# Performance work log

Measured on AMD Instinct MI355X. Metric: run time of the kernel, lower is better.

## Reference

```python
import jax, jax.numpy as jnp
import numpy as np

B, S, H = 4, 256, 768
F = 32            # num_features
T = 256           # TAG_HIDDEN_SIZE
WD = 64           # WIDTH_HIDDEN_SIZE
C = 16            # num_tags


def setup_inputs() -> dict:
    key = jax.random.key(0)
    ks = jax.random.split(key, 10)
    inp = {
        "final_hidden": jax.random.normal(ks[0], (B, S, H), jnp.float32),
        "feature_vecs": jax.random.normal(ks[1], (B, S, F), jnp.float32),
        # Linear params stored [in, out] (transposed vs torch; same math)
        "start_W": jax.random.normal(ks[2], (H + F, T), jnp.float32) * (1.0 / np.sqrt(H + F)),
        "start_b": jnp.zeros((T,), jnp.float32),
        "end_W": jax.random.normal(ks[3], (H + F, T), jnp.float32) * (1.0 / np.sqrt(H + F)),
        "end_b": jnp.zeros((T,), jnp.float32),
        "U": jax.random.normal(ks[4], (T, C, T), jnp.float32) * (1.0 / np.sqrt(T)),
        "width_hidden": jax.random.uniform(ks[5], (S, S, WD), jnp.float32),
        "lin_W": jax.random.normal(ks[6], (2 * T + WD, C), jnp.float32) * (1.0 / np.sqrt(2 * T + WD)),
        "lin_b": jnp.zeros((C,), jnp.float32),
    }
    return inp


def reference(final_hidden, feature_vecs, start_W, start_b, end_W, end_b, U, width_hidden, lin_W, lin_b):
    # dropout p=0.0 -> identity
    x = jnp.concatenate([final_hidden, feature_vecs], axis=-1)   # [B,S,H+F]
    s = x @ start_W + start_b                                    # [B,S,T]
    e = x @ end_W + end_b                                        # [B,S,T]

    # biaffine term: einsum('bsh,hci->bsci') then ('bsci,bei->bsec')
    sU = jnp.einsum('bst,tcu->bscu', s, U)                       # [B,S,C,T]
    pre = jnp.einsum('bscu,beu->bsec', sU, e)                    # [B,S,S,C]

    # pairwise FFN, fused: Linear over concat(start, end, width) decomposes
    # into three small matmuls + broadcast adds (same math, no O(S^2*(2T+W)) buffer)
    Ws, We, Ww = lin_W[:T], lin_W[T:2 * T], lin_W[2 * T:]
    ffn = (jnp.einsum('bst,tc->bsc', s, Ws)[:, :, None, :]
           + jnp.einsum('bet,tc->bec', e, We)[:, None, :, :]
           + jnp.einsum('sew,wc->sec', width_hidden, Ww)[None]
           + lin_b)                                              # [B,S,S,C]
    return pre + ffn
```

## Files before the change

### kernel.cpp

```cpp
#include <hip/hip_runtime.h>


#define B_ 4
#define S_ 256
#define H_ 768
#define F_ 32
#define T_ 256
#define C_ 16
#define R_ 1024
#define HF 800

typedef unsigned short u16;
typedef __attribute__((ext_vector_type(8))) short short8;
typedef __attribute__((ext_vector_type(4))) float f32x4;

__device__ __forceinline__ u16 f2b(float x) {
    unsigned u = __builtin_bit_cast(unsigned, x);
    u += 0x7FFF + ((u >> 16) & 1);
    return (u16)(u >> 16);
}
__device__ __forceinline__ float b2f(u16 b) {
    unsigned u = ((unsigned)b) << 16;
    return __builtin_bit_cast(float, u);
}
__device__ __forceinline__ short8 cvt8(float4 a, float4 b) {
    short8 r;
    r[0] = (short)f2b(a.x); r[1] = (short)f2b(a.y);
    r[2] = (short)f2b(a.z); r[3] = (short)f2b(a.w);
    r[4] = (short)f2b(b.x); r[5] = (short)f2b(b.y);
    r[6] = (short)f2b(b.z); r[7] = (short)f2b(b.w);
    return r;
}

template<int K, int LDA, int LDB, int MF, int NF, int UNROLL>
__device__ __forceinline__ void core(const u16* __restrict__ A,
                                     const u16* __restrict__ B,
                                     int lr, int kgl, f32x4 acc[MF][NF])
{
    const u16* ap[MF];
    const u16* bp[NF];
#pragma unroll
    for (int i = 0; i < MF; ++i) ap[i] = A + (size_t)(i * 16 + lr) * LDA + kgl * 8;
#pragma unroll
    for (int j = 0; j < NF; ++j) bp[j] = B + (size_t)(j * 16 + lr) * LDB + kgl * 8;

#pragma unroll UNROLL
    for (int k = 0; k < K; k += 32) {
        short8 a[MF], b[NF];
#pragma unroll
        for (int i = 0; i < MF; ++i) a[i] = *(const short8*)(ap[i] + k);
#pragma unroll
        for (int j = 0; j < NF; ++j) b[j] = *(const short8*)(bp[j] + k);
#pragma unroll
        for (int i = 0; i < MF; ++i)
#pragma unroll
            for (int j = 0; j < NF; ++j)
                acc[i][j] = __builtin_amdgcn_mfma_f32_16x16x32_bf16(a[i], b[j], acc[i][j], 0, 0, 0);
    }
}

__global__ __launch_bounds__(256)
void k_cvtw(const float* __restrict__ sW, const float* __restrict__ eW,
            u16* __restrict__ Wt)
{
    __shared__ float t_[32][33];
    const int bid = blockIdx.x;
    const int tid = threadIdx.x;
    int k0 = (bid / 16) * 32;
    int j0 = (bid % 16) * 32;
    const float* src = (j0 < T_) ? sW : eW;
    const int js = (j0 < T_) ? j0 : j0 - T_;
    {
        int jl = tid & 31, kl0 = (tid >> 5) * 4;
#pragma unroll
        for (int i = 0; i < 4; ++i)
            t_[kl0 + i][jl] = src[(k0 + kl0 + i) * T_ + js + jl];
    }
    __syncthreads();
    {
        int kl = tid & 31, jl0 = (tid >> 5) * 4;
#pragma unroll
        for (int i = 0; i < 4; ++i)
            Wt[(size_t)(j0 + jl0 + i) * HF + k0 + kl] = f2b(t_[kl][jl0 + i]);
    }
}

__global__ __launch_bounds__(256)
void k_se_cvtu_wc(const float* __restrict__ fh, const float* __restrict__ fv,
                  const u16* __restrict__ Wt,
                  const float* __restrict__ sb, const float* __restrict__ eb,
                  const float* __restrict__ U,
                  const float* __restrict__ linW, const float* __restrict__ linb,
                  const float* __restrict__ WH,
                  u16* __restrict__ SEb, u16* __restrict__ Ut,
                  float* __restrict__ WC)
{
    const int bid = blockIdx.x;
    const int tid = threadIdx.x;

    if (bid < 128) {
        const int l = tid & 63, w = tid >> 6;
        const int wr = w >> 1, wc = w & 1;
        const int lr = l & 15, kgl = l >> 4;
        const int bm = (bid >> 4) * 64;
        const int bn = (bid & 15) * 64;
        f32x4 acc[2][2] = {};

        const u16* aw0 = Wt + (size_t)(bm + wr * 32 + lr) * HF + kgl * 8;
        const u16* aw1 = aw0 + (size_t)16 * HF;
        const float* xr0 = fh + (size_t)(bn + wc * 32 + lr) * H_ + kgl * 8;
        const float* xr1 = xr0 + (size_t)16 * H_;

#pragma unroll 4
        for (int k = 0; k < 768; k += 32) {
            short8 a0 = *(const short8*)(aw0 + k);
            short8 a1 = *(const short8*)(aw1 + k);
            float4 p0 = *(const float4*)(xr0 + k);
            float4 p1 = *(const float4*)(xr0 + k + 4);
            float4 q0 = *(const float4*)(xr1 + k);
            float4 q1 = *(const float4*)(xr1 + k + 4);
            short8 b0 = cvt8(p0, p1);
            short8 b1 = cvt8(q0, q1);
            acc[0][0] = __builtin_amdgcn_mfma_f32_16x16x32_bf16(a0, b0, acc[0][0], 0, 0, 0);
            acc[0][1] = __builtin_amdgcn_mfma_f32_16x16x32_bf16(a0, b1, acc[0][1], 0, 0, 0);
            acc[1][0] = __builtin_amdgcn_mfma_f32_16x16x32_bf16(a1, b0, acc[1][0], 0, 0, 0);
            acc[1][1] = __builtin_amdgcn_mfma_f32_16x16x32_bf16(a1, b1, acc[1][1], 0, 0, 0);
        }
        {
            short8 a0 = *(const short8*)(aw0 + 768);
            short8 a1 = *(const short8*)(aw1 + 768);
            const float* v0 = fv + (size_t)(bn + wc * 32 + lr) * F_ + kgl * 8;
            const float* v1 = v0 + (size_t)16 * F_;
            short8 b0 = cvt8(*(const float4*)v0, *(const float4*)(v0 + 4));
            short8 b1 = cvt8(*(const float4*)v1, *(const float4*)(v1 + 4));
            acc[0][0] = __builtin_amdgcn_mfma_f32_16x16x32_bf16(a0, b0, acc[0][0], 0, 0, 0);
            acc[0][1] = __builtin_amdgcn_mfma_f32_16x16x32_bf16(a0, b1, acc[0][1], 0, 0, 0);
            acc[1][0] = __builtin_amdgcn_mfma_f32_16x16x32_bf16(a1, b0, acc[1][0], 0, 0, 0);
            acc[1][1] = __builtin_amdgcn_mfma_f32_16x16x32_bf16(a1, b1, acc[1][1], 0, 0, 0);
        }

#pragma unroll
        for (int i = 0; i < 2; ++i) {
            int j0 = bm + wr * 32 + i * 16 + kgl * 4;
            float4 bias = (j0 < T_) ? *(const float4*)&sb[j0]
                                    : *(const float4*)&eb[j0 - T_];
#pragma unroll
            for (int jj = 0; jj < 2; ++jj) {
                int r = bn + wc * 32 + jj * 16 + lr;
                ushort4 o;
                o.x = f2b(acc[i][jj][0] + bias.x);
                o.y = f2b(acc[i][jj][1] + bias.y);
                o.z = f2b(acc[i][jj][2] + bias.z);
                o.w = f2b(acc[i][jj][3] + bias.w);
                *(ushort4*)&SEb[(size_t)r * 512 + j0] = o;
            }
        }
        return;
    }
    if (bid < 1152) {
        __shared__ float t_[32][33];
        int bid2 = bid - 128;
        int cu0 = (bid2 >> 3) * 32;
        int t0  = (bid2 & 7) * 32;
        {
            int cul = tid & 31, tl0 = (tid >> 5) * 4;
#pragma unroll
            for (int i = 0; i < 4; ++i)
                t_[tl0 + i][cul] = U[(size_t)(t0 + tl0 + i) * 4096 + cu0 + cul];
        }
        __syncthreads();
        {
            int tl = tid & 31, cul0 = (tid >> 5) * 4;
#pragma unroll
            for (int i = 0; i < 4; ++i)
                Ut[(size_t)(cu0 + cul0 + i) * T_ + t0 + tl] = f2b(t_[tl][cul0 + i]);
        }
        return;
    }
    {
        __shared__ float Wl[16][64];
        __shared__ float Wwl[64][16];
        const int se0 = (bid - 1152) * 128;
        {
            int w0 = tid >> 2, c4 = tid & 3;
            *(float4*)&Wwl[w0][c4 * 4] = *(const float4*)&linW[(512 + w0) * 16 + c4 * 4];
        }
        const int sel = tid >> 4, c = tid & 15;
        const float lb = linb[c];
#pragma unroll
        for (int it = 0; it < 8; ++it) {
            __syncthreads();
            {
                int w4 = tid & 15;
                *(float4*)&Wl[sel][w4 * 4] =
                    *(const float4*)&WH[(size_t)(se0 + it * 16 + sel) * 64 + w4 * 4];
            }
            __syncthreads();
            float acc = lb;
#pragma unroll
            for (int w0 = 0; w0 < 64; ++w0)
                acc += Wl[sel][w0] * Wwl[w0][c];
            WC[(size_t)(se0 + it * 16 + sel) * 16 + c] = acc;
        }
    }
}

__global__ __launch_bounds__(256)
void k_su_scec(const u16* __restrict__ SEb, const u16* __restrict__ Ut,
               const float* __restrict__ linW,
               u16* __restrict__ SUb, float* __restrict__ SCEC)
{
    const int bid = blockIdx.x;
    const int tid = threadIdx.x;

    if (bid < 256) {
        const int l = tid & 63, w = tid >> 6;
        const int wcu = w & 1, wr2 = w >> 1;
        const int lr = l & 15, kgl = l >> 4;
        const int bm = (bid & 31) * 128;
        const int bn = (bid >> 5) * 128;
        f32x4 acc[4][4] = {};

        core<T_, T_, 512, 4, 4, 2>(Ut + (size_t)(bm + wcu * 64) * T_,
                                   SEb + (size_t)(bn + wr2 * 64) * 512,
                                   lr, kgl, acc);

#pragma unroll
        for (int i = 0; i < 4; ++i) {
            int cu0 = bm + wcu * 64 + i * 16 + kgl * 4;
#pragma unroll
            for (int j = 0; j < 4; ++j) {
                int r = bn + wr2 * 64 + j * 16 + lr;
                ushort4 o;
                o.x = f2b(acc[i][j][0]); o.y = f2b(acc[i][j][1]);
                o.z = f2b(acc[i][j][2]); o.w = f2b(acc[i][j][3]);
                *(ushort4*)&SUb[(size_t)r * 4096 + cu0] = o;
            }
        }
        return;
    }
    {
        __shared__ float SEl[4][512];
        const int r0 = (bid - 256) * 4;
#pragma unroll
        for (int i = 0; i < 2; ++i) {
            int ch = tid + i * 256;
            int rl = ch >> 7, o4 = (ch & 127) * 4;
            ushort4 v = *(const ushort4*)&SEb[(size_t)(r0 + rl) * 512 + o4];
            SEl[rl][o4 + 0] = b2f(v.x); SEl[rl][o4 + 1] = b2f(v.y);
            SEl[rl][o4 + 2] = b2f(v.z); SEl[rl][o4 + 3] = b2f(v.w);
        }
        __syncthreads();
        const int rl = tid >> 6, tq = (tid >> 4) & 3, c = tid & 15;
        const int t0 = tq * 64;
        float accs = 0.f, acce = 0.f;
#pragma unroll 4
        for (int t = t0; t < t0 + 64; ++t) {
            accs += SEl[rl][t]       * linW[t * 16 + c];
            acce += SEl[rl][256 + t] * linW[(256 + t) * 16 + c];
        }
        accs += __shfl_xor(accs, 16); accs += __shfl_xor(accs, 32);
        acce += __shfl_xor(acce, 16); acce += __shfl_xor(acce, 32);
        if (tq == 0) {
            SCEC[(r0 + rl) * 32 + c]      = accs;
            SCEC[(r0 + rl) * 32 + 16 + c] = acce;
        }
    }
}

__global__ __launch_bounds__(256)
void k_pre(const u16* __restrict__ SEb, const u16* __restrict__ SUb,
           const float* __restrict__ SCEC, const float* __restrict__ WC,
           float* __restrict__ OUT)
{
    const int bid = blockIdx.x;
    const int tid = threadIdx.x;
    const int n_idx = bid >> 3;
    const int b  = (bid >> 1) & 3;
    const int e_idx = bid & 1;
    const int bm = n_idx * 64;
    const int bn = e_idx * 128;
    const int l = tid & 63, w = tid >> 6;
    const int wn = w >> 1, we = w & 1;
    const int lr = l & 15, kgl = l >> 4;
    f32x4 acc[2][4] = {};

    const u16* An = SUb + ((size_t)b << 20) + (size_t)(bm + wn * 32) * T_;
    const u16* Be = SEb + (size_t)(b << 8) * 512 + 256 + (size_t)(bn + we * 64) * 512;

    core<T_, T_, 512, 2, 4, 4>(An, Be, lr, kgl, acc);

    const int c0 = kgl * 4;
#pragma unroll
    for (int i = 0; i < 2; ++i) {
        int n0 = bm + wn * 32 + i * 16;
        int s = n0 >> 4;
        float4 scv = *(const float4*)&SCEC[((b << 8) + s) * 32 + c0];
#pragma unroll
        for (int j = 0; j < 4; ++j) {
            int e = bn + we * 64 + j * 16 + lr;
            float4 ecv = *(const float4*)&SCEC[((b << 8) + e) * 32 + 16 + c0];
            float4 wcv = *(const float4*)&WC[(size_t)(s * S_ + e) * 16 + c0];
            float4 o;
            o.x = acc[i][j][0] + scv.x + ecv.x + wcv.x;
            o.y = acc[i][j][1] + scv.y + ecv.y + wcv.y;
            o.z = acc[i][j][2] + scv.z + ecv.z + wcv.z;
            o.w = acc[i][j][3] + scv.w + ecv.w + wcv.w;
            *(float4*)&OUT[(((size_t)(b << 8) + s) * S_ + e) * 16 + c0] = o;
        }
    }
}

extern "C" void kernel_launch(void* const* d_in, const int* in_sizes, int n_in,
                              void* d_out, int out_size, void* d_ws, size_t ws_size,
                              hipStream_t stream)
{
    const float* fh   = (const float*)d_in[0];
    const float* fv   = (const float*)d_in[1];
    const float* sW   = (const float*)d_in[2];
    const float* sb   = (const float*)d_in[3];
    const float* eW   = (const float*)d_in[4];
    const float* eb   = (const float*)d_in[5];
    const float* U    = (const float*)d_in[6];
    const float* WH   = (const float*)d_in[7];
    const float* linW = (const float*)d_in[8];
    const float* linb = (const float*)d_in[9];
    float* OUT = (float*)d_out;

    char* p = (char*)d_ws;
    u16* SUb = (u16*)p;      p += (size_t)B_ * 4096 * 256 * 2;
    float* WC = (float*)p;   p += (size_t)S_ * S_ * C_ * 4;
    u16* Ut  = (u16*)p;      p += (size_t)4096 * T_ * 2;
    u16* Wt  = (u16*)p;      p += (size_t)512 * HF * 2;
    u16* SEb = (u16*)p;      p += (size_t)R_ * 512 * 2;
    float* SCEC = (float*)p; p += (size_t)R_ * 32 * 4;

    k_cvtw<<<dim3(400), 256, 0, stream>>>(sW, eW, Wt);
    k_se_cvtu_wc<<<dim3(1664), 256, 0, stream>>>(fh, fv, Wt, sb, eb, U,
                                                 linW, linb, WH, SEb, Ut, WC);
    k_su_scec<<<dim3(512), 256, 0, stream>>>(SEb, Ut, linW, SUb, SCEC);
    k_pre<<<dim3(512), 256, 0, stream>>>(SEb, SUb, SCEC, WC, OUT);
}
```

Before: 62.01 us.

## Fuse weight transpose-convert into projection GEMM and interleave SU/SCEC blocks

Removes the separate k_cvtw launch that transposed and converted start/end weights to bf16. The projection GEMM now reads the fp32 weights directly with strided scalar loads and converts them in registers. It also interleaves the SU GEMM blocks and the SCEC blocks by block-index parity so the heavy and light work mix across the GPU instead of running in two separate phases. This saves a kernel launch and a workspace round trip, at the cost of uncoalesced strided weight loads inside the GEMM inner loop.

```diff
diff --git a/kernel.cpp b/kernel.cpp
--- a/kernel.cpp
+++ b/kernel.cpp
@@ -8,7 +8,6 @@
 #define T_ 256
 #define C_ 16
 #define R_ 1024
-#define HF 800
 
 typedef unsigned short u16;
 typedef __attribute__((ext_vector_type(8))) short short8;
@@ -31,6 +30,12 @@
     r[6] = (short)f2b(b.z); r[7] = (short)f2b(b.w);
     return r;
 }
+__device__ __forceinline__ short8 cvt8p(const float* t) {
+    short8 r;
+#pragma unroll
+    for (int i = 0; i < 8; ++i) r[i] = (short)f2b(t[i]);
+    return r;
+}
 
 template<int K, int LDA, int LDB, int MF, int NF, int UNROLL>
 __device__ __forceinline__ void core(const u16* __restrict__ A,
@@ -60,34 +65,8 @@
 }
 
 __global__ __launch_bounds__(256)
-void k_cvtw(const float* __restrict__ sW, const float* __restrict__ eW,
-            u16* __restrict__ Wt)
-{
-    __shared__ float t_[32][33];
-    const int bid = blockIdx.x;
-    const int tid = threadIdx.x;
-    int k0 = (bid / 16) * 32;
-    int j0 = (bid % 16) * 32;
-    const float* src = (j0 < T_) ? sW : eW;
-    const int js = (j0 < T_) ? j0 : j0 - T_;
-    {
-        int jl = tid & 31, kl0 = (tid >> 5) * 4;
-#pragma unroll
-        for (int i = 0; i < 4; ++i)
-            t_[kl0 + i][jl] = src[(k0 + kl0 + i) * T_ + js + jl];
-    }
-    __syncthreads();
-    {
-        int kl = tid & 31, jl0 = (tid >> 5) * 4;
-#pragma unroll
-        for (int i = 0; i < 4; ++i)
-            Wt[(size_t)(j0 + jl0 + i) * HF + k0 + kl] = f2b(t_[kl][jl0 + i]);
-    }
-}
-
-__global__ __launch_bounds__(256)
 void k_se_cvtu_wc(const float* __restrict__ fh, const float* __restrict__ fv,
-                  const u16* __restrict__ Wt,
+                  const float* __restrict__ sW, const float* __restrict__ eW,
                   const float* __restrict__ sb, const float* __restrict__ eb,
                   const float* __restrict__ U,
                   const float* __restrict__ linW, const float* __restrict__ linb,
@@ -106,19 +85,28 @@
         const int bn = (bid & 15) * 64;
         f32x4 acc[2][2] = {};
 
-        const u16* aw0 = Wt + (size_t)(bm + wr * 32 + lr) * HF + kgl * 8;
-        const u16* aw1 = aw0 + (size_t)16 * HF;
+        const float* srcW = (bm < T_) ? sW : eW;
+        const int js = (bm < T_) ? bm : bm - T_;
+        const int jA0 = js + wr * 32 + lr;
+        const int jA1 = jA0 + 16;
         const float* xr0 = fh + (size_t)(bn + wc * 32 + lr) * H_ + kgl * 8;
         const float* xr1 = xr0 + (size_t)16 * H_;
 
-#pragma unroll 4
-        for (int k = 0; k < 768; k += 32) {
-            short8 a0 = *(const short8*)(aw0 + k);
-            short8 a1 = *(const short8*)(aw1 + k);
-            float4 p0 = *(const float4*)(xr0 + k);
-            float4 p1 = *(const float4*)(xr0 + k + 4);
-            float4 q0 = *(const float4*)(xr1 + k);
-            float4 q1 = *(const float4*)(xr1 + k + 4);
+#pragma unroll 2
+        for (int k0 = 0; k0 < 768; k0 += 32) {
+            float t0[8], t1[8];
+#pragma unroll
+            for (int i = 0; i < 8; ++i) {
+                int krow = k0 + kgl * 8 + i;
+                t0[i] = srcW[(size_t)krow * T_ + jA0];
+                t1[i] = srcW[(size_t)krow * T_ + jA1];
+            }
+            short8 a0 = cvt8p(t0);
+            short8 a1 = cvt8p(t1);
+            float4 p0 = *(const float4*)(xr0 + k0);
+            float4 p1 = *(const float4*)(xr0 + k0 + 4);
+            float4 q0 = *(const float4*)(xr1 + k0);
+            float4 q1 = *(const float4*)(xr1 + k0 + 4);
             short8 b0 = cvt8(p0, p1);
             short8 b1 = cvt8(q0, q1);
             acc[0][0] = __builtin_amdgcn_mfma_f32_16x16x32_bf16(a0, b0, acc[0][0], 0, 0, 0);
@@ -127,8 +115,15 @@
             acc[1][1] = __builtin_amdgcn_mfma_f32_16x16x32_bf16(a1, b1, acc[1][1], 0, 0, 0);
         }
         {
-            short8 a0 = *(const short8*)(aw0 + 768);
-            short8 a1 = *(const short8*)(aw1 + 768);
+            float t0[8], t1[8];
+#pragma unroll
+            for (int i = 0; i < 8; ++i) {
+                int krow = 768 + kgl * 8 + i;
+                t0[i] = srcW[(size_t)krow * T_ + jA0];
+                t1[i] = srcW[(size_t)krow * T_ + jA1];
+            }
+            short8 a0 = cvt8p(t0);
+            short8 a1 = cvt8p(t1);
             const float* v0 = fv + (size_t)(bn + wc * 32 + lr) * F_ + kgl * 8;
             const float* v1 = v0 + (size_t)16 * F_;
             short8 b0 = cvt8(*(const float4*)v0, *(const float4*)(v0 + 4));
@@ -213,12 +208,13 @@
     const int bid = blockIdx.x;
     const int tid = threadIdx.x;
 
-    if (bid < 256) {
+    if (!(bid & 1)) {
+        const int idx = bid >> 1;
         const int l = tid & 63, w = tid >> 6;
         const int wcu = w & 1, wr2 = w >> 1;
         const int lr = l & 15, kgl = l >> 4;
-        const int bm = (bid & 31) * 128;
-        const int bn = (bid >> 5) * 128;
+        const int bm = (idx & 31) * 128;
+        const int bn = (idx >> 5) * 128;
         f32x4 acc[4][4] = {};
 
         core<T_, T_, 512, 4, 4, 2>(Ut + (size_t)(bm + wcu * 64) * T_,
@@ -241,7 +237,7 @@
     }
     {
         __shared__ float SEl[4][512];
-        const int r0 = (bid - 256) * 4;
+        const int r0 = (bid >> 1) * 4;
 #pragma unroll
         for (int i = 0; i < 2; ++i) {
             int ch = tid + i * 256;
@@ -331,12 +327,10 @@
     u16* SUb = (u16*)p;      p += (size_t)B_ * 4096 * 256 * 2;
     float* WC = (float*)p;   p += (size_t)S_ * S_ * C_ * 4;
     u16* Ut  = (u16*)p;      p += (size_t)4096 * T_ * 2;
-    u16* Wt  = (u16*)p;      p += (size_t)512 * HF * 2;
     u16* SEb = (u16*)p;      p += (size_t)R_ * 512 * 2;
     float* SCEC = (float*)p; p += (size_t)R_ * 32 * 4;
 
-    k_cvtw<<<dim3(400), 256, 0, stream>>>(sW, eW, Wt);
-    k_se_cvtu_wc<<<dim3(1664), 256, 0, stream>>>(fh, fv, Wt, sb, eb, U,
+    k_se_cvtu_wc<<<dim3(1664), 256, 0, stream>>>(fh, fv, sW, eW, sb, eb, U,
                                                  linW, linb, WH, SEb, Ut, WC);
     k_su_scec<<<dim3(512), 256, 0, stream>>>(SEb, Ut, linW, SUb, SCEC);
     k_pre<<<dim3(512), 256, 0, stream>>>(SEb, SUb, SCEC, WC, OUT);
```

Result: slower. 65.10 us (+5.0%).

## Merge four kernel launches into one persistent kernel with grid barriers

Applied to the files above, without the earlier changes.

Combines the weight-convert, projection, SU/SCEC and final biaffine stages into a single persistent kernel of 512 blocks separated by atomic-counter grid barriers, with the old conversion blocks distributed as a job loop. The goal is to remove per-launch overhead and inter-kernel gaps. In exchange it adds a memset launch, spin-wait barriers that require all 512 blocks to be co-resident, and it leaves some blocks idle during the stages with fewer work items.

```diff
diff --git a/kernel.cpp b/kernel.cpp
--- a/kernel.cpp
+++ b/kernel.cpp
@@ -9,8 +9,10 @@
 #define C_ 16
 #define R_ 1024
 #define HF 800
+#define NBLK 512
 
 typedef unsigned short u16;
+typedef unsigned int u32;
 typedef __attribute__((ext_vector_type(8))) short short8;
 typedef __attribute__((ext_vector_type(4))) float f32x4;
 
@@ -32,6 +34,25 @@
     return r;
 }
 
+__device__ __forceinline__ void gbar(u32* bar, int idx, int nb) {
+    __syncthreads();
+    if (threadIdx.x == 0) {
+        u32* cnt = bar + idx * 64;
+        u32* flg = bar + idx * 64 + 32;
+        __threadfence();
+        u32 old = atomicAdd(cnt, 1u);
+        if (old == (u32)(nb - 1)) {
+            __threadfence();
+            __hip_atomic_store(flg, 1u, __ATOMIC_RELAXED, __HIP_MEMORY_SCOPE_AGENT);
+        } else {
+            while (__hip_atomic_load(flg, __ATOMIC_RELAXED, __HIP_MEMORY_SCOPE_AGENT) == 0u)
+                __builtin_amdgcn_s_sleep(8);
+            __threadfence();
+        }
+    }
+    __syncthreads();
+}
+
 template<int K, int LDA, int LDB, int MF, int NF, int UNROLL>
 __device__ __forceinline__ void core(const u16* __restrict__ A,
                                      const u16* __restrict__ B,
@@ -59,44 +80,104 @@
     }
 }
 
-__global__ __launch_bounds__(256)
-void k_cvtw(const float* __restrict__ sW, const float* __restrict__ eW,
-            u16* __restrict__ Wt)
-{
-    __shared__ float t_[32][33];
+__device__ void cvtw_job(int job, int tid, const float* __restrict__ sW,
+                         const float* __restrict__ eW, u16* __restrict__ Wt,
+                         float* sh)
+{
+    float (*t_)[33] = (float(*)[33])sh;
+    int k0 = (job / 16) * 32;
+    int j0 = (job % 16) * 32;
+    const float* src = (j0 < T_) ? sW : eW;
+    const int js = (j0 < T_) ? j0 : j0 - T_;
+    {
+        int jl = tid & 31, kl0 = (tid >> 5) * 4;
+#pragma unroll
+        for (int i = 0; i < 4; ++i)
+            t_[kl0 + i][jl] = src[(k0 + kl0 + i) * T_ + js + jl];
+    }
+    __syncthreads();
+    {
+        int kl = tid & 31, jl0 = (tid >> 5) * 4;
+#pragma unroll
+        for (int i = 0; i < 4; ++i)
+            Wt[(size_t)(j0 + jl0 + i) * HF + k0 + kl] = f2b(t_[kl][jl0 + i]);
+    }
+    __syncthreads();
+}
+
+__device__ void cvtu_job(int job, int tid, const float* __restrict__ U,
+                         u16* __restrict__ Ut, float* sh)
+{
+    float (*t_)[33] = (float(*)[33])sh;
+    int cu0 = (job >> 3) * 32;
+    int t0  = (job & 7) * 32;
+    {
+        int cul = tid & 31, tl0 = (tid >> 5) * 4;
+#pragma unroll
+        for (int i = 0; i < 4; ++i)
+            t_[tl0 + i][cul] = U[(size_t)(t0 + tl0 + i) * 4096 + cu0 + cul];
+    }
+    __syncthreads();
+    {
+        int tl = tid & 31, cul0 = (tid >> 5) * 4;
+#pragma unroll
+        for (int i = 0; i < 4; ++i)
+            Ut[(size_t)(cu0 + cul0 + i) * T_ + t0 + tl] = f2b(t_[tl][cul0 + i]);
+    }
+    __syncthreads();
+}
+
+__device__ void wc_job(int job, int tid, const float* __restrict__ WH,
+                       const float* __restrict__ linW, const float* __restrict__ linb,
+                       float* __restrict__ WC, float* sh)
+{
+    float* Wl  = sh;
+    float* Wwl = sh + 1024;
+    const int se0 = job * 128;
+    {
+        int w0 = tid >> 2, c4 = tid & 3;
+        *(float4*)&Wwl[w0 * 16 + c4 * 4] = *(const float4*)&linW[(512 + w0) * 16 + c4 * 4];
+    }
+    const int sel = tid >> 4, c = tid & 15;
+    const float lb = linb[c];
+#pragma unroll
+    for (int it = 0; it < 8; ++it) {
+        __syncthreads();
+        {
+            int w4 = tid & 15;
+            *(float4*)&Wl[sel * 64 + w4 * 4] =
+                *(const float4*)&WH[(size_t)(se0 + it * 16 + sel) * 64 + w4 * 4];
+        }
+        __syncthreads();
+        float acc = lb;
+#pragma unroll
+        for (int w0 = 0; w0 < 64; ++w0)
+            acc += Wl[sel * 64 + w0] * Wwl[w0 * 16 + c];
+        WC[(size_t)(se0 + it * 16 + sel) * 16 + c] = acc;
+    }
+    __syncthreads();
+}
+
+__global__ __launch_bounds__(256, 2)
+void k_mega(const float* __restrict__ fh, const float* __restrict__ fv,
+            const float* __restrict__ sW, const float* __restrict__ sb,
+            const float* __restrict__ eW, const float* __restrict__ eb,
+            const float* __restrict__ U,  const float* __restrict__ WH,
+            const float* __restrict__ linW, const float* __restrict__ linb,
+            u16* __restrict__ Wt, u16* __restrict__ Ut, float* __restrict__ WC,
+            u16* __restrict__ SEb, float* __restrict__ SCEC,
+            u16* __restrict__ SUb, float* __restrict__ OUT, u32* bar)
+{
+    __shared__ float sh[2112];
     const int bid = blockIdx.x;
     const int tid = threadIdx.x;
-    int k0 = (bid / 16) * 32;
-    int j0 = (bid % 16) * 32;
-    const float* src = (j0 < T_) ? sW : eW;
-    const int js = (j0 < T_) ? j0 : j0 - T_;
-    {
-        int jl = tid & 31, kl0 = (tid >> 5) * 4;
-#pragma unroll
-        for (int i = 0; i < 4; ++i)
-            t_[kl0 + i][jl] = src[(k0 + kl0 + i) * T_ + js + jl];
-    }
-    __syncthreads();
-    {
-        int kl = tid & 31, jl0 = (tid >> 5) * 4;
-#pragma unroll
-        for (int i = 0; i < 4; ++i)
-            Wt[(size_t)(j0 + jl0 + i) * HF + k0 + kl] = f2b(t_[kl][jl0 + i]);
-    }
-}
-
-__global__ __launch_bounds__(256)
-void k_se_cvtu_wc(const float* __restrict__ fh, const float* __restrict__ fv,
-                  const u16* __restrict__ Wt,
-                  const float* __restrict__ sb, const float* __restrict__ eb,
-                  const float* __restrict__ U,
-                  const float* __restrict__ linW, const float* __restrict__ linb,
-                  const float* __restrict__ WH,
-                  u16* __restrict__ SEb, u16* __restrict__ Ut,
-                  float* __restrict__ WC)
-{
-    const int bid = blockIdx.x;
-    const int tid = threadIdx.x;
+
+    for (int job = bid; job < 1936; job += NBLK) {
+        if (job < 400)       cvtw_job(job, tid, sW, eW, Wt, sh);
+        else if (job < 1424) cvtu_job(job - 400, tid, U, Ut, sh);
+        else                 wc_job(job - 1424, tid, WH, linW, linb, WC, sh);
+    }
+    gbar(bar, 0, NBLK);
 
     if (bid < 128) {
         const int l = tid & 63, w = tid >> 6;
@@ -155,70 +236,16 @@
                 *(ushort4*)&SEb[(size_t)r * 512 + j0] = o;
             }
         }
-        return;
-    }
-    if (bid < 1152) {
-        __shared__ float t_[32][33];
-        int bid2 = bid - 128;
-        int cu0 = (bid2 >> 3) * 32;
-        int t0  = (bid2 & 7) * 32;
-        {
-            int cul = tid & 31, tl0 = (tid >> 5) * 4;
-#pragma unroll
-            for (int i = 0; i < 4; ++i)
-                t_[tl0 + i][cul] = U[(size_t)(t0 + tl0 + i) * 4096 + cu0 + cul];
-        }
-        __syncthreads();
-        {
-            int tl = tid & 31, cul0 = (tid >> 5) * 4;
-#pragma unroll
-            for (int i = 0; i < 4; ++i)
-                Ut[(size_t)(cu0 + cul0 + i) * T_ + t0 + tl] = f2b(t_[tl][cul0 + i]);
-        }
-        return;
-    }
-    {
-        __shared__ float Wl[16][64];
-        __shared__ float Wwl[64][16];
-        const int se0 = (bid - 1152) * 128;
-        {
-            int w0 = tid >> 2, c4 = tid & 3;
-            *(float4*)&Wwl[w0][c4 * 4] = *(const float4*)&linW[(512 + w0) * 16 + c4 * 4];
-        }
-        const int sel = tid >> 4, c = tid & 15;
-        const float lb = linb[c];
-#pragma unroll
-        for (int it = 0; it < 8; ++it) {
-            __syncthreads();
-            {
-                int w4 = tid & 15;
-                *(float4*)&Wl[sel][w4 * 4] =
-                    *(const float4*)&WH[(size_t)(se0 + it * 16 + sel) * 64 + w4 * 4];
-            }
-            __syncthreads();
-            float acc = lb;
-#pragma unroll
-            for (int w0 = 0; w0 < 64; ++w0)
-                acc += Wl[sel][w0] * Wwl[w0][c];
-            WC[(size_t)(se0 + it * 16 + sel) * 16 + c] = acc;
-        }
-    }
-}
-
-__global__ __launch_bounds__(256)
-void k_su_scec(const u16* __restrict__ SEb, const u16* __restrict__ Ut,
-               const float* __restrict__ linW,
-               u16* __restrict__ SUb, float* __restrict__ SCEC)
-{
-    const int bid = blockIdx.x;
-    const int tid = threadIdx.x;
-
-    if (bid < 256) {
+    }
+    gbar(bar, 1, NBLK);
+
+    if (!(bid & 1)) {
+        const int idx = bid >> 1;
         const int l = tid & 63, w = tid >> 6;
         const int wcu = w & 1, wr2 = w >> 1;
         const int lr = l & 15, kgl = l >> 4;
-        const int bm = (bid & 31) * 128;
-        const int bn = (bid >> 5) * 128;
+        const int bm = (idx & 31) * 128;
+        const int bn = (idx >> 5) * 128;
         f32x4 acc[4][4] = {};
 
         core<T_, T_, 512, 4, 4, 2>(Ut + (size_t)(bm + wcu * 64) * T_,
@@ -237,18 +264,16 @@
                 *(ushort4*)&SUb[(size_t)r * 4096 + cu0] = o;
             }
         }
-        return;
-    }
-    {
-        __shared__ float SEl[4][512];
-        const int r0 = (bid - 256) * 4;
+    } else {
+        float* SEl = sh;
+        const int r0 = (bid >> 1) * 4;
 #pragma unroll
         for (int i = 0; i < 2; ++i) {
             int ch = tid + i * 256;
             int rl = ch >> 7, o4 = (ch & 127) * 4;
             ushort4 v = *(const ushort4*)&SEb[(size_t)(r0 + rl) * 512 + o4];
-            SEl[rl][o4 + 0] = b2f(v.x); SEl[rl][o4 + 1] = b2f(v.y);
-            SEl[rl][o4 + 2] = b2f(v.z); SEl[rl][o4 + 3] = b2f(v.w);
+            SEl[rl * 512 + o4 + 0] = b2f(v.x); SEl[rl * 512 + o4 + 1] = b2f(v.y);
+            SEl[rl * 512 + o4 + 2] = b2f(v.z); SEl[rl * 512 + o4 + 3] = b2f(v.w);
         }
         __syncthreads();
         const int rl = tid >> 6, tq = (tid >> 4) & 3, c = tid & 15;
@@ -256,8 +281,8 @@
         float accs = 0.f, acce = 0.f;
 #pragma unroll 4
         for (int t = t0; t < t0 + 64; ++t) {
-            accs += SEl[rl][t]       * linW[t * 16 + c];
-            acce += SEl[rl][256 + t] * linW[(256 + t) * 16 + c];
+            accs += SEl[rl * 512 + t]       * linW[t * 16 + c];
+            acce += SEl[rl * 512 + 256 + t] * linW[(256 + t) * 16 + c];
         }
         accs += __shfl_xor(accs, 16); accs += __shfl_xor(accs, 32);
         acce += __shfl_xor(acce, 16); acce += __shfl_xor(acce, 32);
@@ -265,48 +290,44 @@
             SCEC[(r0 + rl) * 32 + c]      = accs;
             SCEC[(r0 + rl) * 32 + 16 + c] = acce;
         }
-    }
-}
-
-__global__ __launch_bounds__(256)
-void k_pre(const u16* __restrict__ SEb, const u16* __restrict__ SUb,
-           const float* __restrict__ SCEC, const float* __restrict__ WC,
-           float* __restrict__ OUT)
-{
-    const int bid = blockIdx.x;
-    const int tid = threadIdx.x;
-    const int n_idx = bid >> 3;
-    const int b  = (bid >> 1) & 3;
-    const int e_idx = bid & 1;
-    const int bm = n_idx * 64;
-    const int bn = e_idx * 128;
-    const int l = tid & 63, w = tid >> 6;
-    const int wn = w >> 1, we = w & 1;
-    const int lr = l & 15, kgl = l >> 4;
-    f32x4 acc[2][4] = {};
-
-    const u16* An = SUb + ((size_t)b << 20) + (size_t)(bm + wn * 32) * T_;
-    const u16* Be = SEb + (size_t)(b << 8) * 512 + 256 + (size_t)(bn + we * 64) * 512;
-
-    core<T_, T_, 512, 2, 4, 4>(An, Be, lr, kgl, acc);
-
-    const int c0 = kgl * 4;
-#pragma unroll
-    for (int i = 0; i < 2; ++i) {
-        int n0 = bm + wn * 32 + i * 16;
-        int s = n0 >> 4;
-        float4 scv = *(const float4*)&SCEC[((b << 8) + s) * 32 + c0];
-#pragma unroll
-        for (int j = 0; j < 4; ++j) {
-            int e = bn + we * 64 + j * 16 + lr;
-            float4 ecv = *(const float4*)&SCEC[((b << 8) + e) * 32 + 16 + c0];
-            float4 wcv = *(const float4*)&WC[(size_t)(s * S_ + e) * 16 + c0];
-            float4 o;
-            o.x = acc[i][j][0] + scv.x + ecv.x + wcv.x;
-            o.y = acc[i][j][1] + scv.y + ecv.y + wcv.y;
-            o.z = acc[i][j][2] + scv.z + ecv.z + wcv.z;
-            o.w = acc[i][j][3] + scv.w + ecv.w + wcv.w;
-            *(float4*)&OUT[(((size_t)(b << 8) + s) * S_ + e) * 16 + c0] = o;
+        __syncthreads();
+    }
+    gbar(bar, 2, NBLK);
+
+    {
+        const int n_idx = bid >> 3;
+        const int b  = (bid >> 1) & 3;
+        const int e_idx = bid & 1;
+        const int bm = n_idx * 64;
+        const int bn = e_idx * 128;
+        const int l = tid & 63, w = tid >> 6;
+        const int wn = w >> 1, we = w & 1;
+        const int lr = l & 15, kgl = l >> 4;
+        f32x4 acc[2][4] = {};
+
+        const u16* An = SUb + ((size_t)b << 20) + (size_t)(bm + wn * 32) * T_;
+        const u16* Be = SEb + (size_t)(b << 8) * 512 + 256 + (size_t)(bn + we * 64) * 512;
+
+        core<T_, T_, 512, 2, 4, 4>(An, Be, lr, kgl, acc);
+
+        const int c0 = kgl * 4;
+#pragma unroll
+        for (int i = 0; i < 2; ++i) {
+            int n0 = bm + wn * 32 + i * 16;
+            int s = n0 >> 4;
+            float4 scv = *(const float4*)&SCEC[((b << 8) + s) * 32 + c0];
+#pragma unroll
+            for (int j = 0; j < 4; ++j) {
+                int e = bn + we * 64 + j * 16 + lr;
+                float4 ecv = *(const float4*)&SCEC[((b << 8) + e) * 32 + 16 + c0];
+                float4 wcv = *(const float4*)&WC[(size_t)(s * S_ + e) * 16 + c0];
+                float4 o;
+                o.x = acc[i][j][0] + scv.x + ecv.x + wcv.x;
+                o.y = acc[i][j][1] + scv.y + ecv.y + wcv.y;
+                o.z = acc[i][j][2] + scv.z + ecv.z + wcv.z;
+                o.w = acc[i][j][3] + scv.w + ecv.w + wcv.w;
+                *(float4*)&OUT[(((size_t)(b << 8) + s) * S_ + e) * 16 + c0] = o;
+            }
         }
     }
 }
@@ -334,10 +355,10 @@
     u16* Wt  = (u16*)p;      p += (size_t)512 * HF * 2;
     u16* SEb = (u16*)p;      p += (size_t)R_ * 512 * 2;
     float* SCEC = (float*)p; p += (size_t)R_ * 32 * 4;
-
-    k_cvtw<<<dim3(400), 256, 0, stream>>>(sW, eW, Wt);
-    k_se_cvtu_wc<<<dim3(1664), 256, 0, stream>>>(fh, fv, Wt, sb, eb, U,
-                                                 linW, linb, WH, SEb, Ut, WC);
-    k_su_scec<<<dim3(512), 256, 0, stream>>>(SEb, Ut, linW, SUb, SCEC);
-    k_pre<<<dim3(512), 256, 0, stream>>>(SEb, SUb, SCEC, WC, OUT);
-}
+    u32* bar = (u32*)p;      p += 1024;
+
+    hipMemsetAsync(bar, 0, 1024, stream);
+    k_mega<<<dim3(NBLK), 256, 0, stream>>>(fh, fv, sW, sb, eW, eb, U, WH,
+                                           linW, linb, Wt, Ut, WC, SEb, SCEC,
+                                           SUb, OUT, bar);
+}
```

Measured after the change: 142.9 us. 130% more time.
